# Kernel optimization log

Hardware: AMD Instinct MI355X
Metric: run time of the kernel (lower is better)

The kernel has to match this reference:

```python
import jax, jax.numpy as jnp
import numpy as np

DIM, HEAD, FFN = 256, 4, 1024
NEG = -1e9


def layer_norm(x, g, b, eps=1e-5):
    mu = jnp.mean(x, axis=-1, keepdims=True)
    var = jnp.mean((x - mu) ** 2, axis=-1, keepdims=True)
    return (x - mu) / jnp.sqrt(var + eps) * g + b


def setup_inputs() -> dict:
    key = jax.random.key(0)
    ks = jax.random.split(key, 10)
    B, T, D = 8, 2048, DIM
    s = 1.0 / np.sqrt(D)
    x = jax.random.normal(ks[0], (B, T, D), dtype=jnp.float32)
    mask = jax.random.randint(ks[1], (B, T), 0, 2).astype(jnp.float32)
    Wqkv = jax.random.uniform(ks[2], (3 * D, D), jnp.float32, -s, s)
    bqkv = jnp.zeros((3 * D,), jnp.float32)
    Wo = jax.random.uniform(ks[3], (D, D), jnp.float32, -s, s)
    bo = jnp.zeros((D,), jnp.float32)
    W1 = jax.random.uniform(ks[4], (FFN, D), jnp.float32, -s, s)
    b1 = jnp.zeros((FFN,), jnp.float32)
    W2 = jax.random.uniform(ks[5], (D, FFN), jnp.float32, -1.0 / np.sqrt(FFN), 1.0 / np.sqrt(FFN))
    b2 = jnp.zeros((D,), jnp.float32)
    g1 = jnp.ones((D,), jnp.float32); be1 = jnp.zeros((D,), jnp.float32)
    g2 = jnp.ones((D,), jnp.float32); be2 = jnp.zeros((D,), jnp.float32)
    return dict(x=x, mask=mask, Wqkv=Wqkv, bqkv=bqkv, Wo=Wo, bo=bo,
                W1=W1, b1=b1, W2=W2, b2=b2, g1=g1, be1=be1, g2=g2, be2=be2)


def _forward(x, mask, Wqkv, bqkv, Wo, bo, W1, b1, W2, b2, g1, be1, g2, be2):
    B, T, D = x.shape
    H = HEAD
    hd = D // H
    # --- MultiheadAttention (explicit, non-flash path, need_weights=True) ---
    qkv = jnp.einsum('btd,ed->bte', x, Wqkv) + bqkv            # (B,T,3D)
    q, k, v = jnp.split(qkv, 3, axis=-1)
    q = q.reshape(B, T, H, hd).transpose(0, 2, 1, 3)           # (B,H,T,hd)
    k = k.reshape(B, T, H, hd).transpose(0, 2, 1, 3)
    v = v.reshape(B, T, H, hd).transpose(0, 2, 1, 3)
    scores = jnp.einsum('bhqd,bhkd->bhqk', q, k) / jnp.sqrt(jnp.float32(hd))
    scores = jnp.where(mask[:, None, None, :] > 0.5, NEG, scores)
    w = jax.nn.softmax(scores, axis=-1)                        # (B,H,T,T)
    attn = jnp.einsum('bhqk,bhkd->bhqd', w, v)                 # (B,H,T,hd)
    attn = attn.transpose(0, 2, 1, 3).reshape(B, T, D)
    attn_out = jnp.einsum('btd,ed->bte', attn, Wo) + bo        # (B,T,D)
    w_avg = jnp.mean(w, axis=1)                                # (B,T,T), averaged over heads
    # halting score: sum over query dim (dim=1), then masked softmax
    halting = jnp.sum(w_avg, axis=1)                           # (B,T)
    halting = jax.nn.softmax(halting + mask * (-1e10), axis=-1)
    # --- residual + LN + FFN + LN ---
    h = layer_norm(x + attn_out, g1, be1)
    ffn = jnp.einsum('btf,df->btd', jax.nn.relu(jnp.einsum('btd,fd->btf', h, W1) + b1), W2) + b2
    out = layer_norm(h + ffn, g2, be2)
    return out, halting


def reference(x, mask, Wqkv, bqkv, Wo, bo, W1, b1, W2, b2, g1, be1, g2, be2):
    return _forward(x, mask, Wqkv, bqkv, Wo, bo, W1, b1, W2, b2, g1, be1, g2, be2)
```

## Files before the change

### kernel.cpp

```cpp
#include <hip/hip_runtime.h>
#include <hip/hip_bf16.h>
#include <math.h>

namespace {

constexpr int B = 8, T = 2048, D = 256, H = 4, HD = 64, FF = 1024;
constexpr float QSCALE = 0.18033688f;

typedef __attribute__((ext_vector_type(8))) short short8;
typedef __attribute__((ext_vector_type(4))) short s16x4;
typedef __attribute__((ext_vector_type(4))) float f32x4;

__device__ __forceinline__ short f2bf(float f) {
    __hip_bfloat16 h = __float2bfloat16(f);
    return *reinterpret_cast<short*>(&h);
}
__device__ __forceinline__ float exp2a(float x) {
    float r; asm("v_exp_f32 %0, %1" : "=v"(r) : "v"(x)); return r;
}
__device__ __forceinline__ unsigned cvtpk(float lo, float hi) {
    unsigned r; asm("v_cvt_pk_bf16_f32 %0, %1, %2" : "=v"(r) : "v"(lo), "v"(hi)); return r;
}
__device__ __forceinline__ void gload16(const void* g, void* l) {
    __builtin_amdgcn_global_load_lds(
        (const __attribute__((address_space(1))) void*)g,
        (__attribute__((address_space(3))) void*)l, 16, 0, 0);
}

__global__ __launch_bounds__(256) void k_cvt(
        const float* __restrict__ x,  const float* __restrict__ wq,
        const float* __restrict__ wo, const float* __restrict__ w1,
        const float* __restrict__ w2,
        short* __restrict__ x16,  short* __restrict__ wq16,
        short* __restrict__ wo16, short* __restrict__ w116,
        short* __restrict__ w216) {
    const int N0 = 524288, N1 = 24576, N2 = 8192, N3 = 32768, N4 = 32768;
    const int total = N0 + N1 + N2 + N3 + N4;
    for (int i = blockIdx.x*256 + threadIdx.x; i < total; i += gridDim.x*256) {
        const float* s; short* d; int j = i;
        if (j < N0) { s = x; d = x16; }
        else { j -= N0;
            if (j < N1) { s = wq; d = wq16; }
            else { j -= N1;
                if (j < N2) { s = wo; d = wo16; }
                else { j -= N2;
                    if (j < N3) { s = w1; d = w116; }
                    else { j -= N3; s = w2; d = w216; }
                }
            }
        }
        float4 a = ((const float4*)s)[j*2], b2 = ((const float4*)s)[j*2+1];
        short8 o;
        o[0]=f2bf(a.x);  o[1]=f2bf(a.y);  o[2]=f2bf(a.z);  o[3]=f2bf(a.w);
        o[4]=f2bf(b2.x); o[5]=f2bf(b2.y); o[6]=f2bf(b2.z); o[7]=f2bf(b2.w);
        ((short8*)d)[j] = o;
    }
}

template<int MODE>
__global__ __launch_bounds__(256) void k_gemm128(
        const short* __restrict__ A, const short* __restrict__ W,
        const float* __restrict__ bias, const int K,
        short* __restrict__ oq, short* __restrict__ ok, short* __restrict__ ov,
        short* __restrict__ o16) {
    __shared__ char pool[34048];
    short* Asl = (short*)pool;
    short* Wsl = (short*)(pool + 16384);
    float (*Cs)[133] = (float(*)[133])pool;

    const int tid = threadIdx.x;
    const int w = tid >> 6, lane = tid & 63;
    const int qr = lane & 15, g = lane >> 4;
    const int wm = w >> 1, wn = w & 1;
    const int m0 = blockIdx.x * 128;
    const int n0 = blockIdx.y * 128;
    const int srow = lane >> 3;
    const int scb  = (lane & 7) ^ srow;

    f32x4 acc[4][4];
    #pragma unroll
    for (int i = 0; i < 4; i++)
        #pragma unroll
        for (int j = 0; j < 4; j++) acc[i][j] = (f32x4){0.f, 0.f, 0.f, 0.f};

    for (int k0 = 0; k0 < K; k0 += 64) {
        __syncthreads();
        #pragma unroll
        for (int i = 0; i < 4; i++) {
            const int chunk = i*4 + w;
            const int row = chunk*8 + srow;
            gload16(A + (size_t)(m0 + row)*K + k0 + scb*8, Asl + chunk*512);
            gload16(W + (size_t)(n0 + row)*K + k0 + scb*8, Wsl + chunk*512);
        }
        __syncthreads();
        #pragma unroll
        for (int kk = 0; kk < 2; kk++) {
            const int swz = ((g + 4*kk) ^ (qr & 7)) * 8;
            short8 af[4], bf[4];
            #pragma unroll
            for (int fm = 0; fm < 4; fm++)
                af[fm] = *(const short8*)(Asl + (wm*64 + fm*16 + qr)*64 + swz);
            #pragma unroll
            for (int fn = 0; fn < 4; fn++)
                bf[fn] = *(const short8*)(Wsl + (wn*64 + fn*16 + qr)*64 + swz);
            #pragma unroll
            for (int fm = 0; fm < 4; fm++)
                #pragma unroll
                for (int fn = 0; fn < 4; fn++)
                    acc[fm][fn] = __builtin_amdgcn_mfma_f32_16x16x32_bf16(
                        af[fm], bf[fn], acc[fm][fn], 0, 0, 0);
        }
    }

    const int b = m0 >> 11;
    const int tl0 = m0 & (T - 1);

    if (MODE == 0 && blockIdx.y >= 4) {
        #pragma unroll
        for (int fm = 0; fm < 4; fm++) {
            const int tl = tl0 + wm*64 + fm*16 + g*4;
            #pragma unroll
            for (int fn = 0; fn < 4; fn++) {
                const int nv = (n0 - 512) + wn*64 + fn*16 + qr;
                const int h = nv >> 6, d = nv & 63;
                const float bv = bias[n0 + wn*64 + fn*16 + qr];
                s16x4 pk;
                #pragma unroll
                for (int r = 0; r < 4; r++) pk[r] = f2bf(acc[fm][fn][r] + bv);
                *(s16x4*)&ov[((size_t)(b*H + h)*HD + d)*T + tl] = pk;
            }
        }
        return;
    }

    __syncthreads();
    const int erow = tid & 63, c0 = (tid >> 6) * 32;
    #pragma unroll
    for (int hh = 0; hh < 2; hh++) {
        if (wm == hh) {
            #pragma unroll
            for (int fm = 0; fm < 4; fm++)
                #pragma unroll
                for (int fn = 0; fn < 4; fn++)
                    #pragma unroll
                    for (int r = 0; r < 4; r++)
                        Cs[fm*16 + g*4 + r][wn*64 + fn*16 + qr] = acc[fm][fn][r];
        }
        __syncthreads();
        float vals[32];
        #pragma unroll
        for (int j = 0; j < 32; j++) vals[j] = Cs[erow][c0 + j] + bias[n0 + c0 + j];
        const int tl = tl0 + hh*64 + erow;
        if (MODE == 0) {
            const int by = blockIdx.y;
            short* dst = (by < 2) ? oq : ok;
            const float qs = (by < 2) ? QSCALE : 1.0f;
            const int h = (by & 1)*2 + (c0 >> 6);
            const int d0 = c0 & 63;
            short8 s0, s1, s2, s3;
            #pragma unroll
            for (int j = 0; j < 8; j++) {
                s0[j] = f2bf(vals[j]*qs);
                s1[j] = f2bf(vals[8+j]*qs);
                s2[j] = f2bf(vals[16+j]*qs);
                s3[j] = f2bf(vals[24+j]*qs);
            }
            short* p = dst + ((size_t)(b*H + h)*T + tl)*HD + d0;
            *(short8*)p = s0;
            *(short8*)(p + 8) = s1;
            *(short8*)(p + 16) = s2;
            *(short8*)(p + 24) = s3;
        } else {
            short8 s0, s1, s2, s3;
            #pragma unroll
            for (int j = 0; j < 8; j++) {
                s0[j] = f2bf(fmaxf(vals[j],    0.f));
                s1[j] = f2bf(fmaxf(vals[8+j],  0.f));
                s2[j] = f2bf(fmaxf(vals[16+j], 0.f));
                s3[j] = f2bf(fmaxf(vals[24+j], 0.f));
            }
            short* p = o16 + (size_t)(m0 + hh*64 + erow)*1024 + n0 + c0;
            *(short8*)p = s0;
            *(short8*)(p + 8) = s1;
            *(short8*)(p + 16) = s2;
            *(short8*)(p + 24) = s3;
        }
        if (hh == 0) __syncthreads();
    }
}

template<int MODE>
__global__ __launch_bounds__(256) void k_gemm(
        const short* __restrict__ A, const short* __restrict__ W,
        const float* __restrict__ bias, const int K,
        float* __restrict__ of) {
    __shared__ short As[64][72];
    __shared__ short Ws[64][72];
    __shared__ float Cs[64][68];
    const int tid = threadIdx.x;
    const int w = tid >> 6, lane = tid & 63;
    const int qr = lane & 15, g = lane >> 4;
    const int wm = w >> 1, wn = w & 1;
    const int m0 = blockIdx.x * 64;
    const int n0 = blockIdx.y * 64;
    const int srow = tid >> 2, scol = (tid & 3) * 8;
    const short* Ag = A + (size_t)(m0 + srow) * K + scol;
    const short* Wg = W + (size_t)(n0 + srow) * K + scol;

    f32x4 acc[2][2];
    #pragma unroll
    for (int i = 0; i < 2; i++)
        #pragma unroll
        for (int j = 0; j < 2; j++) acc[i][j] = (f32x4){0.f, 0.f, 0.f, 0.f};

    for (int k0 = 0; k0 < K; k0 += 64) {
        __syncthreads();
        *(short8*)&As[srow][scol]      = *(const short8*)(Ag + k0);
        *(short8*)&As[srow][scol + 32] = *(const short8*)(Ag + k0 + 32);
        *(short8*)&Ws[srow][scol]      = *(const short8*)(Wg + k0);
        *(short8*)&Ws[srow][scol + 32] = *(const short8*)(Wg + k0 + 32);
        __syncthreads();
        #pragma unroll
        for (int kk = 0; kk < 2; kk++) {
            short8 a0 = *(const short8*)&As[wm*32 + qr][g*8 + kk*32];
            short8 a1 = *(const short8*)&As[wm*32 + 16 + qr][g*8 + kk*32];
            short8 b0 = *(const short8*)&Ws[wn*32 + qr][g*8 + kk*32];
            short8 b1 = *(const short8*)&Ws[wn*32 + 16 + qr][g*8 + kk*32];
            acc[0][0] = __builtin_amdgcn_mfma_f32_16x16x32_bf16(a0, b0, acc[0][0], 0, 0, 0);
            acc[0][1] = __builtin_amdgcn_mfma_f32_16x16x32_bf16(a0, b1, acc[0][1], 0, 0, 0);
            acc[1][0] = __builtin_amdgcn_mfma_f32_16x16x32_bf16(a1, b0, acc[1][0], 0, 0, 0);
            acc[1][1] = __builtin_amdgcn_mfma_f32_16x16x32_bf16(a1, b1, acc[1][1], 0, 0, 0);
        }
    }

    #pragma unroll
    for (int fm = 0; fm < 2; fm++)
        #pragma unroll
        for (int fn = 0; fn < 2; fn++)
            #pragma unroll
            for (int r = 0; r < 4; r++)
                Cs[wm*32 + fm*16 + g*4 + r][wn*32 + fn*16 + qr] = acc[fm][fn][r];
    __syncthreads();
    const int row = tid >> 2, c0 = (tid & 3) * 16;
    float vals[16];
    #pragma unroll
    for (int j = 0; j < 16; j++) vals[j] = Cs[row][c0 + j] + bias[n0 + c0 + j];
    float* p = of + (size_t)(m0 + row)*256 + n0 + c0;
    #pragma unroll
    for (int jj = 0; jj < 4; jj++) *(float4*)(p + jj*4) = *(float4*)&vals[jj*4];
}

__global__ __launch_bounds__(256) void k_flashL(
        const short* __restrict__ qb, const short* __restrict__ kb,
        const float* __restrict__ mask, float* __restrict__ liout) {
    __shared__ short Ks[128][72];
    __shared__ float lbuf[4][4][16];
    const int tid = threadIdx.x;
    const int w = tid >> 6, lane = tid & 63;
    const int qr = lane & 15, g = lane >> 4;
    const int qt = blockIdx.x, h = blockIdx.y, b = blockIdx.z;
    const int bh = b*H + h;
    const int q0 = qt*64;

    short8 qf[4][2];
    {
        const short* qg = qb + ((size_t)bh * T + q0) * HD;
        #pragma unroll
        for (int qt4 = 0; qt4 < 4; qt4++) {
            qf[qt4][0] = *(const short8*)(qg + (qt4*16 + qr)*HD + g*8);
            qf[qt4][1] = *(const short8*)(qg + (qt4*16 + qr)*HD + 32 + g*8);
        }
    }
    const short* kg0 = kb + (size_t)bh * T * HD;
    const float* mg  = mask + (size_t)b * T;
    const int krow = lane >> 1, khalf = (lane & 1) * 32;

    float lrun[4] = {0.f, 0.f, 0.f, 0.f};

    short8 kreg[4];
    #pragma unroll
    for (int c = 0; c < 4; c++)
        kreg[c] = *(const short8*)(kg0 + (size_t)(w*32 + krow)*HD + khalf + c*8);
    #pragma unroll
    for (int c = 0; c < 4; c++)
        *(short8*)&Ks[w*32 + krow][khalf + c*8] = kreg[c];
    asm volatile("" ::: "memory");

    for (int kt = 0; kt < 16; kt++) {
        const int kbase = kt*128 + w*32;
        if (kt < 15) {
            const int nb = (kt+1)*128 + w*32;
            #pragma unroll
            for (int c = 0; c < 4; c++)
                kreg[c] = *(const short8*)(kg0 + (size_t)(nb + krow)*HD + khalf + c*8);
        }
        #pragma unroll
        for (int kt2 = 0; kt2 < 2; kt2++) {
            short8 kf0 = *(const short8*)&Ks[w*32 + kt2*16 + qr][g*8];
            short8 kf1 = *(const short8*)&Ks[w*32 + kt2*16 + qr][g*8 + 32];
            const int key0 = kbase + kt2*16;
            const float4 mv4 = *(const float4*)(mg + key0 + 4*g);
            const float b0 = (mv4.x > 0.5f) ? -1e9f : 0.f;
            const float b1 = (mv4.y > 0.5f) ? -1e9f : 0.f;
            const float b2v = (mv4.z > 0.5f) ? -1e9f : 0.f;
            const float b3 = (mv4.w > 0.5f) ? -1e9f : 0.f;
            #pragma unroll
            for (int qt4 = 0; qt4 < 4; qt4++) {
                f32x4 sa = (f32x4){b0, b1, b2v, b3};
                sa = __builtin_amdgcn_mfma_f32_16x16x32_bf16(kf0, qf[qt4][0], sa, 0, 0, 0);
                sa = __builtin_amdgcn_mfma_f32_16x16x32_bf16(kf1, qf[qt4][1], sa, 0, 0, 0);
                lrun[qt4] += (exp2a(sa[0]) + exp2a(sa[1])) + (exp2a(sa[2]) + exp2a(sa[3]));
            }
        }
        if (kt < 15) {
            asm volatile("" ::: "memory");
            #pragma unroll
            for (int c = 0; c < 4; c++)
                *(short8*)&Ks[w*32 + krow][khalf + c*8] = kreg[c];
            asm volatile("" ::: "memory");
        }
    }
    #pragma unroll
    for (int qt4 = 0; qt4 < 4; qt4++) {
        lrun[qt4] += __shfl_xor(lrun[qt4], 16, 64);
        lrun[qt4] += __shfl_xor(lrun[qt4], 32, 64);
    }
    if (g == 0) {
        #pragma unroll
        for (int qt4 = 0; qt4 < 4; qt4++) lbuf[w][qt4][qr] = lrun[qt4];
    }
    __syncthreads();
    if (tid < 64) {
        const int qt4 = tid >> 4, qrr = tid & 15;
        const float l = lbuf[0][qt4][qrr] + lbuf[1][qt4][qrr]
                      + lbuf[2][qt4][qrr] + lbuf[3][qt4][qrr];
        liout[(size_t)bh*T + q0 + tid] = -__log2f(l);
    }
}

__global__ __launch_bounds__(256) void k_fattn(
        const short* __restrict__ qb, const short* __restrict__ kb,
        const short* __restrict__ vtb, const float* __restrict__ mask,
        const float* __restrict__ liout,
        short* __restrict__ attnb, float* __restrict__ part4) {
    __shared__ short Ks[128][68];
    __shared__ short Vt[64][132];
    __shared__ short Ps[4][64][36];
    const int tid = threadIdx.x;
    const int w = tid >> 6, lane = tid & 63;
    const int qr = lane & 15, g = lane >> 4;
    const int qt = blockIdx.x, h = blockIdx.y, b = blockIdx.z;
    const int bh = b*H + h;
    const int q0 = qt*64;

    short8 qf[4][2];
    float li[4];
    {
        const short* qg = qb + ((size_t)bh * T + q0) * HD;
        #pragma unroll
        for (int qt4 = 0; qt4 < 4; qt4++) {
            qf[qt4][0] = *(const short8*)(qg + (qt4*16 + qr)*HD + g*8);
            qf[qt4][1] = *(const short8*)(qg + (qt4*16 + qr)*HD + 32 + g*8);
            li[qt4] = liout[(size_t)bh*T + q0 + qt4*16 + qr];
        }
    }
    const short* kg0 = kb + (size_t)bh * T * HD;
    const short* vg0 = vtb + (size_t)bh * HD * T;
    const float* mg  = mask + (size_t)b * T;
    float* csrow = part4 + (size_t)(bh*32 + qt) * T;
    const int krow = lane >> 1, khalf = (lane & 1) * 32;

    f32x4 oa[4][4];
    #pragma unroll
    for (int nt = 0; nt < 4; nt++)
        #pragma unroll
        for (int qt4 = 0; qt4 < 4; qt4++) oa[nt][qt4] = (f32x4){0.f,0.f,0.f,0.f};

    short8 kreg[4], vreg[4];
    #pragma unroll
    for (int c = 0; c < 4; c++) {
        kreg[c] = *(const short8*)(kg0 + (size_t)(w*32 + krow)*HD + khalf + c*8);
        vreg[c] = *(const short8*)(vg0 + (size_t)lane*T + w*32 + c*8);
    }
    #pragma unroll
    for (int c = 0; c < 4; c++) {
        *(short8*)&Ks[w*32 + krow][khalf + c*8] = kreg[c];
        *(short8*)&Vt[lane][w*32 + c*8] = vreg[c];
    }
    asm volatile("" ::: "memory");

    for (int kt = 0; kt < 16; kt++) {
        if (kt < 15) {
            const int nb = (kt+1)*128 + w*32;
            #pragma unroll
            for (int c = 0; c < 4; c++) {
                kreg[c] = *(const short8*)(kg0 + (size_t)(nb + krow)*HD + khalf + c*8);
                vreg[c] = *(const short8*)(vg0 + (size_t)lane*T + nb + c*8);
            }
        }
        const int kbase = kt*128 + w*32;
        #pragma unroll
        for (int kt2 = 0; kt2 < 2; kt2++) {
            short8 kf0 = *(const short8*)&Ks[w*32 + kt2*16 + qr][g*8];
            short8 kf1 = *(const short8*)&Ks[w*32 + kt2*16 + qr][g*8 + 32];
            const int key0 = kbase + kt2*16;
            const float4 mv4 = *(const float4*)(mg + key0 + 4*g);
            const float mb[4] = { (mv4.x > 0.5f) ? -1e9f : 0.f,
                                  (mv4.y > 0.5f) ? -1e9f : 0.f,
                                  (mv4.z > 0.5f) ? -1e9f : 0.f,
                                  (mv4.w > 0.5f) ? -1e9f : 0.f };
            float p[4][4];
            #pragma unroll
            for (int qt4 = 0; qt4 < 4; qt4++) {
                f32x4 sa = (f32x4){mb[0] + li[qt4], mb[1] + li[qt4],
                                   mb[2] + li[qt4], mb[3] + li[qt4]};
                sa = __builtin_amdgcn_mfma_f32_16x16x32_bf16(kf0, qf[qt4][0], sa, 0, 0, 0);
                sa = __builtin_amdgcn_mfma_f32_16x16x32_bf16(kf1, qf[qt4][1], sa, 0, 0, 0);
                p[qt4][0] = exp2a(sa[0]); p[qt4][1] = exp2a(sa[1]);
                p[qt4][2] = exp2a(sa[2]); p[qt4][3] = exp2a(sa[3]);
            }
            float cs[4];
            #pragma unroll
            for (int r = 0; r < 4; r++) {
                cs[r] = (p[0][r] + p[1][r]) + (p[2][r] + p[3][r]);
                cs[r] += __shfl_xor(cs[r], 1, 64);
                cs[r] += __shfl_xor(cs[r], 2, 64);
                cs[r] += __shfl_xor(cs[r], 4, 64);
                cs[r] += __shfl_xor(cs[r], 8, 64);
            }
            if (qr == 0) {
                #pragma unroll
                for (int r = 0; r < 4; r++) csrow[key0 + 4*g + r] = cs[r];
            }
            #pragma unroll
            for (int qt4 = 0; qt4 < 4; qt4++) {
                union { unsigned u[2]; s16x4 s; } cv;
                cv.u[0] = cvtpk(p[qt4][0], p[qt4][1]);
                cv.u[1] = cvtpk(p[qt4][2], p[qt4][3]);
                *(s16x4*)&Ps[w][qt4*16 + qr][kt2*16 + 4*g] = cv.s;
            }
        }
        asm volatile("" ::: "memory");
        short8 pa[4];
        #pragma unroll
        for (int qt4 = 0; qt4 < 4; qt4++)
            pa[qt4] = *(const short8*)&Ps[w][qt4*16 + qr][g*8];
        #pragma unroll
        for (int nt = 0; nt < 4; nt++) {
            short8 vf = *(const short8*)&Vt[nt*16 + qr][w*32 + g*8];
            #pragma unroll
            for (int qt4 = 0; qt4 < 4; qt4++)
                oa[nt][qt4] = __builtin_amdgcn_mfma_f32_16x16x32_bf16(vf, pa[qt4], oa[nt][qt4], 0, 0, 0);
        }
        if (kt < 15) {
            asm volatile("" ::: "memory");
            #pragma unroll
            for (int c = 0; c < 4; c++) {
                *(short8*)&Ks[w*32 + krow][khalf + c*8] = kreg[c];
                *(short8*)&Vt[lane][w*32 + c*8] = vreg[c];
            }
            asm volatile("" ::: "memory");
        }
    }

    __syncthreads();
    float* Obuf = (float*)&Ks[0][0];
    const int qL = tid >> 2, dq = tid & 3;
    #pragma unroll
    for (int nt = 0; nt < 4; nt++) {
        #pragma unroll
        for (int qt4 = 0; qt4 < 4; qt4++)
            #pragma unroll
            for (int r = 0; r < 4; r++)
                Obuf[(w*16 + 4*g + r)*68 + qt4*16 + qr] = oa[nt][qt4][r];
        __syncthreads();
        s16x4 pk;
        #pragma unroll
        for (int rr = 0; rr < 4; rr++) {
            const int dr = dq*4 + rr;
            float v = Obuf[(0*16 + dr)*68 + qL] + Obuf[(1*16 + dr)*68 + qL]
                    + Obuf[(2*16 + dr)*68 + qL] + Obuf[(3*16 + dr)*68 + qL];
            pk[rr] = f2bf(v);
        }
        *(s16x4*)&attnb[((size_t)b*T + q0 + qL)*D + h*HD + nt*16 + dq*4] = pk;
        __syncthreads();
    }
}

__global__ __launch_bounds__(256) void k_red(
        const float* __restrict__ part, float* __restrict__ red) {
    __shared__ float s[128];
    const int b = blockIdx.y, kc = blockIdx.x;
    const int tid = threadIdx.x;
    const int c = tid & 127, half = tid >> 7;
    const int k = kc*128 + c;
    const float* pb = part + ((size_t)(b*128 + half*64))*T + k;
    float acc = 0.f;
    #pragma unroll 8
    for (int r = 0; r < 64; r++) acc += pb[(size_t)r*T];
    if (half) s[c] = acc;
    __syncthreads();
    if (!half) red[(size_t)b*T + k] = acc + s[c];
}

__global__ __launch_bounds__(256) void k_halt(
        const float* __restrict__ red, const float* __restrict__ mask,
        float* __restrict__ outh) {
    __shared__ float redm[4], reds[4];
    const int b = blockIdx.x, tid = threadIdx.x;
    const float* mg = mask + (size_t)b * T;
    float v[8];
    float M = -3e38f;
    #pragma unroll
    for (int i = 0; i < 8; i++) {
        v[i] = red[(size_t)b*T + tid + i*256]*0.25f + mg[tid + i*256]*(-1e10f);
        M = fmaxf(M, v[i]);
    }
    #pragma unroll
    for (int off = 1; off < 64; off <<= 1) M = fmaxf(M, __shfl_xor(M, off, 64));
    const int wv = tid >> 6, lane = tid & 63;
    if (lane == 0) redm[wv] = M;
    __syncthreads();
    M = fmaxf(fmaxf(redm[0], redm[1]), fmaxf(redm[2], redm[3]));
    float S = 0.f;
    #pragma unroll
    for (int i = 0; i < 8; i++) { v[i] = __expf(v[i] - M); S += v[i]; }
    #pragma unroll
    for (int off = 1; off < 64; off <<= 1) S += __shfl_xor(S, off, 64);
    if (lane == 0) reds[wv] = S;
    __syncthreads();
    const float invS = 1.f / (reds[0] + reds[1] + reds[2] + reds[3]);
    #pragma unroll
    for (int i = 0; i < 8; i++) outh[(size_t)b*T + tid + i*256] = v[i]*invS;
}

__global__ __launch_bounds__(256) void k_ln(
        const float* __restrict__ a, const float* __restrict__ bsrc,
        const float* __restrict__ g, const float* __restrict__ be,
        float* __restrict__ yf, short* __restrict__ y16) {
    __shared__ float s[16][D];
    const int tid = threadIdx.x;
    const size_t row0 = (size_t)blockIdx.x * 16;
    const float4* ag = (const float4*)(a + row0*D);
    const float4* bg = (const float4*)(bsrc + row0*D);
    #pragma unroll
    for (int i = 0; i < 4; i++) {
        float4 av = ag[tid + i*256], bv = bg[tid + i*256];
        float4 sv = {av.x+bv.x, av.y+bv.y, av.z+bv.z, av.w+bv.w};
        ((float4*)&s[0][0])[tid + i*256] = sv;
    }
    __syncthreads();
    const int wv = tid >> 6, lane = tid & 63;
    float gvv[4], bvv[4];
    #pragma unroll
    for (int s2 = 0; s2 < 4; s2++) { gvv[s2] = g[lane + 64*s2]; bvv[s2] = be[lane + 64*s2]; }
    #pragma unroll
    for (int rr = 0; rr < 4; rr++) {
        const int r = wv*4 + rr;
        float x0 = s[r][lane],     x1 = s[r][lane+64];
        float x2 = s[r][lane+128], x3 = s[r][lane+192];
        float sum = x0+x1+x2+x3;
        float ssq = x0*x0 + x1*x1 + x2*x2 + x3*x3;
        #pragma unroll
        for (int off = 1; off < 64; off <<= 1) {
            sum += __shfl_xor(sum, off, 64);
            ssq += __shfl_xor(ssq, off, 64);
        }
        const float mu = sum * (1.f/256.f);
        const float rs = rsqrtf(ssq*(1.f/256.f) - mu*mu + 1e-5f);
        float y0 = (x0 - mu)*rs*gvv[0] + bvv[0];
        float y1 = (x1 - mu)*rs*gvv[1] + bvv[1];
        float y2 = (x2 - mu)*rs*gvv[2] + bvv[2];
        float y3 = (x3 - mu)*rs*gvv[3] + bvv[3];
        float* yp = yf + (row0 + r)*D;
        yp[lane]     = y0;
        yp[lane+64]  = y1;
        yp[lane+128] = y2;
        yp[lane+192] = y3;
        if (y16) {
            short* hp = y16 + (row0 + r)*D;
            hp[lane]     = f2bf(y0);
            hp[lane+64]  = f2bf(y1);
            hp[lane+128] = f2bf(y2);
            hp[lane+192] = f2bf(y3);
        }
    }
}

}

extern "C" void kernel_launch(void* const* d_in, const int* in_sizes, int n_in,
                              void* d_out, int out_size, void* d_ws, size_t ws_size,
                              hipStream_t stream) {
    (void)in_sizes; (void)n_in; (void)out_size; (void)ws_size;
    const float* x    = (const float*)d_in[0];
    const float* mask = (const float*)d_in[1];
    const float* Wqkv = (const float*)d_in[2];
    const float* bqkv = (const float*)d_in[3];
    const float* Wo   = (const float*)d_in[4];
    const float* bo   = (const float*)d_in[5];
    const float* W1   = (const float*)d_in[6];
    const float* b1   = (const float*)d_in[7];
    const float* W2   = (const float*)d_in[8];
    const float* b2   = (const float*)d_in[9];
    const float* g1   = (const float*)d_in[10];
    const float* be1  = (const float*)d_in[11];
    const float* g2   = (const float*)d_in[12];
    const float* be2  = (const float*)d_in[13];

    float* out  = (float*)d_out;
    char*  wsb  = (char*)d_ws;
    const size_t MB = 1024*1024;

    short* qb16   = (short*)(wsb + 0*MB);
    short* kb16   = (short*)(wsb + 8*MB);
    short* vt16   = (short*)(wsb + 16*MB);
    short* x16    = (short*)(wsb + 24*MB);
    short* attn16 = (short*)(wsb + 24*MB);
    short* mid16  = (short*)(wsb + 0*MB);
    float* part4  = (float*)(wsb + 32*MB);
    float* redb   = (float*)(wsb + 40*MB);
    float* liout  = (float*)(wsb + 41*MB);
    short* wq16   = (short*)(wsb + 42*MB);
    short* wo16   = (short*)(wsb + 42*MB + 393216);
    short* w116   = (short*)(wsb + 42*MB + 524288);
    short* w216   = (short*)(wsb + 42*MB + 1048576);
    float* hb     = (float*)(wsb + 44*MB);
    short* h16    = (short*)(wsb + 60*MB);
    float* po     = (float*)(wsb + 68*MB);
    float* fo     = (float*)(wsb + 68*MB);
    float* outh   = out + (size_t)B*T*D;

    k_cvt      <<<dim3(1024),       256, 0, stream>>>(x, Wqkv, Wo, W1, W2,
                                                      x16, wq16, wo16, w116, w216);
    k_gemm128<0><<<dim3(128, 6),    256, 0, stream>>>(x16, wq16, bqkv, 256,
                                                      qb16, kb16, vt16, nullptr);
    k_flashL   <<<dim3(32, H, B),   256, 0, stream>>>(qb16, kb16, mask, liout);
    k_fattn    <<<dim3(32, H, B),   256, 0, stream>>>(qb16, kb16, vt16, mask, liout,
                                                      attn16, part4);
    k_red      <<<dim3(16, B),      256, 0, stream>>>(part4, redb);
    k_halt     <<<dim3(B),          256, 0, stream>>>(redb, mask, outh);
    k_gemm<1>  <<<dim3(256, 4),     256, 0, stream>>>(attn16, wo16, bo, 256, po);
    k_ln       <<<dim3(B*T/16),     256, 0, stream>>>(x, po, g1, be1, hb, h16);
    k_gemm128<2><<<dim3(128, 8),    256, 0, stream>>>(h16, w116, b1, 256,
                                                      nullptr, nullptr, nullptr, mid16);
    k_gemm<3>  <<<dim3(256, 4),     256, 0, stream>>>(mid16, w216, b2, 1024, fo);
    k_ln       <<<dim3(B*T/16),     256, 0, stream>>>(hb, fo, g2, be2, out, nullptr);
}
```

Measured before the change: 231.9 us.

## Fuse softmax-denominator pass into attention kernel and use 128-tile GEMM for FFN2

Merges the separate row-sum (log-sum-exp) kernel into the attention kernel. Each block now computes its own denominators in a first pass over K, then runs the PV pass without a global round trip for liout and without a second launch. The second FFN GEMM also moves from the 64x64 kernel to the 128x128 tiled kernel through a new fp32 output mode. Risks are higher LDS use and register pressure in the fused attention kernel, and fewer blocks (256) for the FFN2 GEMM.

```diff
diff --git a/kernel.cpp b/kernel.cpp
--- a/kernel.cpp
+++ b/kernel.cpp
@@ -62,7 +62,7 @@
         const short* __restrict__ A, const short* __restrict__ W,
         const float* __restrict__ bias, const int K,
         short* __restrict__ oq, short* __restrict__ ok, short* __restrict__ ov,
-        short* __restrict__ o16) {
+        short* __restrict__ o16, float* __restrict__ ofp) {
     __shared__ char pool[34048];
     short* Asl = (short*)pool;
     short* Wsl = (short*)(pool + 16384);
@@ -170,7 +170,7 @@
             *(short8*)(p + 8) = s1;
             *(short8*)(p + 16) = s2;
             *(short8*)(p + 24) = s3;
-        } else {
+        } else if (MODE == 2) {
             short8 s0, s1, s2, s3;
             #pragma unroll
             for (int j = 0; j < 8; j++) {
@@ -184,6 +184,11 @@
             *(short8*)(p + 8) = s1;
             *(short8*)(p + 16) = s2;
             *(short8*)(p + 24) = s3;
+        } else {
+            float* p = ofp + (size_t)(m0 + hh*64 + erow)*256 + n0 + c0;
+            #pragma unroll
+            for (int jj = 0; jj < 8; jj++)
+                *(float4*)(p + jj*4) = *(float4*)&vals[jj*4];
         }
         if (hh == 0) __syncthreads();
     }
@@ -250,10 +255,13 @@
     for (int jj = 0; jj < 4; jj++) *(float4*)(p + jj*4) = *(float4*)&vals[jj*4];
 }
 
-__global__ __launch_bounds__(256) void k_flashL(
+__global__ __launch_bounds__(256) void k_flatt(
         const short* __restrict__ qb, const short* __restrict__ kb,
-        const float* __restrict__ mask, float* __restrict__ liout) {
-    __shared__ short Ks[128][72];
+        const short* __restrict__ vtb, const float* __restrict__ mask,
+        short* __restrict__ attnb, float* __restrict__ part4) {
+    __shared__ short Ks[128][68];
+    __shared__ short Vt[64][132];
+    __shared__ short Ps[4][64][36];
     __shared__ float lbuf[4][4][16];
     const int tid = threadIdx.x;
     const int w = tid >> 6, lane = tid & 63;
@@ -272,103 +280,75 @@
         }
     }
     const short* kg0 = kb + (size_t)bh * T * HD;
-    const float* mg  = mask + (size_t)b * T;
-    const int krow = lane >> 1, khalf = (lane & 1) * 32;
-
-    float lrun[4] = {0.f, 0.f, 0.f, 0.f};
-
-    short8 kreg[4];
-    #pragma unroll
-    for (int c = 0; c < 4; c++)
-        kreg[c] = *(const short8*)(kg0 + (size_t)(w*32 + krow)*HD + khalf + c*8);
-    #pragma unroll
-    for (int c = 0; c < 4; c++)
-        *(short8*)&Ks[w*32 + krow][khalf + c*8] = kreg[c];
-    asm volatile("" ::: "memory");
-
-    for (int kt = 0; kt < 16; kt++) {
-        const int kbase = kt*128 + w*32;
-        if (kt < 15) {
-            const int nb = (kt+1)*128 + w*32;
-            #pragma unroll
-            for (int c = 0; c < 4; c++)
-                kreg[c] = *(const short8*)(kg0 + (size_t)(nb + krow)*HD + khalf + c*8);
-        }
-        #pragma unroll
-        for (int kt2 = 0; kt2 < 2; kt2++) {
-            short8 kf0 = *(const short8*)&Ks[w*32 + kt2*16 + qr][g*8];
-            short8 kf1 = *(const short8*)&Ks[w*32 + kt2*16 + qr][g*8 + 32];
-            const int key0 = kbase + kt2*16;
-            const float4 mv4 = *(const float4*)(mg + key0 + 4*g);
-            const float b0 = (mv4.x > 0.5f) ? -1e9f : 0.f;
-            const float b1 = (mv4.y > 0.5f) ? -1e9f : 0.f;
-            const float b2v = (mv4.z > 0.5f) ? -1e9f : 0.f;
-            const float b3 = (mv4.w > 0.5f) ? -1e9f : 0.f;
-            #pragma unroll
-            for (int qt4 = 0; qt4 < 4; qt4++) {
-                f32x4 sa = (f32x4){b0, b1, b2v, b3};
-                sa = __builtin_amdgcn_mfma_f32_16x16x32_bf16(kf0, qf[qt4][0], sa, 0, 0, 0);
-                sa = __builtin_amdgcn_mfma_f32_16x16x32_bf16(kf1, qf[qt4][1], sa, 0, 0, 0);
-                lrun[qt4] += (exp2a(sa[0]) + exp2a(sa[1])) + (exp2a(sa[2]) + exp2a(sa[3]));
-            }
-        }
-        if (kt < 15) {
-            asm volatile("" ::: "memory");
-            #pragma unroll
-            for (int c = 0; c < 4; c++)
-                *(short8*)&Ks[w*32 + krow][khalf + c*8] = kreg[c];
-            asm volatile("" ::: "memory");
-        }
-    }
-    #pragma unroll
-    for (int qt4 = 0; qt4 < 4; qt4++) {
-        lrun[qt4] += __shfl_xor(lrun[qt4], 16, 64);
-        lrun[qt4] += __shfl_xor(lrun[qt4], 32, 64);
-    }
-    if (g == 0) {
-        #pragma unroll
-        for (int qt4 = 0; qt4 < 4; qt4++) lbuf[w][qt4][qr] = lrun[qt4];
-    }
-    __syncthreads();
-    if (tid < 64) {
-        const int qt4 = tid >> 4, qrr = tid & 15;
-        const float l = lbuf[0][qt4][qrr] + lbuf[1][qt4][qrr]
-                      + lbuf[2][qt4][qrr] + lbuf[3][qt4][qrr];
-        liout[(size_t)bh*T + q0 + tid] = -__log2f(l);
-    }
-}
-
-__global__ __launch_bounds__(256) void k_fattn(
-        const short* __restrict__ qb, const short* __restrict__ kb,
-        const short* __restrict__ vtb, const float* __restrict__ mask,
-        const float* __restrict__ liout,
-        short* __restrict__ attnb, float* __restrict__ part4) {
-    __shared__ short Ks[128][68];
-    __shared__ short Vt[64][132];
-    __shared__ short Ps[4][64][36];
-    const int tid = threadIdx.x;
-    const int w = tid >> 6, lane = tid & 63;
-    const int qr = lane & 15, g = lane >> 4;
-    const int qt = blockIdx.x, h = blockIdx.y, b = blockIdx.z;
-    const int bh = b*H + h;
-    const int q0 = qt*64;
-
-    short8 qf[4][2];
-    float li[4];
-    {
-        const short* qg = qb + ((size_t)bh * T + q0) * HD;
-        #pragma unroll
-        for (int qt4 = 0; qt4 < 4; qt4++) {
-            qf[qt4][0] = *(const short8*)(qg + (qt4*16 + qr)*HD + g*8);
-            qf[qt4][1] = *(const short8*)(qg + (qt4*16 + qr)*HD + 32 + g*8);
-            li[qt4] = liout[(size_t)bh*T + q0 + qt4*16 + qr];
-        }
-    }
-    const short* kg0 = kb + (size_t)bh * T * HD;
     const short* vg0 = vtb + (size_t)bh * HD * T;
     const float* mg  = mask + (size_t)b * T;
     float* csrow = part4 + (size_t)(bh*32 + qt) * T;
     const int krow = lane >> 1, khalf = (lane & 1) * 32;
+
+    float lrun[4] = {0.f, 0.f, 0.f, 0.f};
+    {
+        short8 kreg[4];
+        #pragma unroll
+        for (int c = 0; c < 4; c++)
+            kreg[c] = *(const short8*)(kg0 + (size_t)(w*32 + krow)*HD + khalf + c*8);
+        #pragma unroll
+        for (int c = 0; c < 4; c++)
+            *(short8*)&Ks[w*32 + krow][khalf + c*8] = kreg[c];
+        asm volatile("" ::: "memory");
+
+        for (int kt = 0; kt < 16; kt++) {
+            const int kbase = kt*128 + w*32;
+            if (kt < 15) {
+                const int nb = (kt+1)*128 + w*32;
+                #pragma unroll
+                for (int c = 0; c < 4; c++)
+                    kreg[c] = *(const short8*)(kg0 + (size_t)(nb + krow)*HD + khalf + c*8);
+            }
+            #pragma unroll
+            for (int kt2 = 0; kt2 < 2; kt2++) {
+                short8 kf0 = *(const short8*)&Ks[w*32 + kt2*16 + qr][g*8];
+                short8 kf1 = *(const short8*)&Ks[w*32 + kt2*16 + qr][g*8 + 32];
+                const int key0 = kbase + kt2*16;
+                const float4 mv4 = *(const float4*)(mg + key0 + 4*g);
+                const float b0 = (mv4.x > 0.5f) ? -1e9f : 0.f;
+                const float b1 = (mv4.y > 0.5f) ? -1e9f : 0.f;
+                const float b2v = (mv4.z > 0.5f) ? -1e9f : 0.f;
+                const float b3 = (mv4.w > 0.5f) ? -1e9f : 0.f;
+                #pragma unroll
+                for (int qt4 = 0; qt4 < 4; qt4++) {
+                    f32x4 sa = (f32x4){b0, b1, b2v, b3};
+                    sa = __builtin_amdgcn_mfma_f32_16x16x32_bf16(kf0, qf[qt4][0], sa, 0, 0, 0);
+                    sa = __builtin_amdgcn_mfma_f32_16x16x32_bf16(kf1, qf[qt4][1], sa, 0, 0, 0);
+                    lrun[qt4] += (exp2a(sa[0]) + exp2a(sa[1])) + (exp2a(sa[2]) + exp2a(sa[3]));
+                }
+            }
+            if (kt < 15) {
+                asm volatile("" ::: "memory");
+                #pragma unroll
+                for (int c = 0; c < 4; c++)
+                    *(short8*)&Ks[w*32 + krow][khalf + c*8] = kreg[c];
+                asm volatile("" ::: "memory");
+            }
+        }
+    }
+    #pragma unroll
+    for (int qt4 = 0; qt4 < 4; qt4++) {
+        lrun[qt4] += __shfl_xor(lrun[qt4], 16, 64);
+        lrun[qt4] += __shfl_xor(lrun[qt4], 32, 64);
+    }
+    if (g == 0) {
+        #pragma unroll
+        for (int qt4 = 0; qt4 < 4; qt4++) lbuf[w][qt4][qr] = lrun[qt4];
+    }
+    __syncthreads();
+    float li[4];
+    #pragma unroll
+    for (int qt4 = 0; qt4 < 4; qt4++) {
+        const float l = lbuf[0][qt4][qr] + lbuf[1][qt4][qr]
+                      + lbuf[2][qt4][qr] + lbuf[3][qt4][qr];
+        li[qt4] = -__log2f(l);
+    }
+    __syncthreads();
 
     f32x4 oa[4][4];
     #pragma unroll
@@ -620,7 +600,6 @@
     short* mid16  = (short*)(wsb + 0*MB);
     float* part4  = (float*)(wsb + 32*MB);
     float* redb   = (float*)(wsb + 40*MB);
-    float* liout  = (float*)(wsb + 41*MB);
     short* wq16   = (short*)(wsb + 42*MB);
     short* wo16   = (short*)(wsb + 42*MB + 393216);
     short* w116   = (short*)(wsb + 42*MB + 524288);
@@ -634,16 +613,16 @@
     k_cvt      <<<dim3(1024),       256, 0, stream>>>(x, Wqkv, Wo, W1, W2,
                                                       x16, wq16, wo16, w116, w216);
     k_gemm128<0><<<dim3(128, 6),    256, 0, stream>>>(x16, wq16, bqkv, 256,
-                                                      qb16, kb16, vt16, nullptr);
-    k_flashL   <<<dim3(32, H, B),   256, 0, stream>>>(qb16, kb16, mask, liout);
-    k_fattn    <<<dim3(32, H, B),   256, 0, stream>>>(qb16, kb16, vt16, mask, liout,
+                                                      qb16, kb16, vt16, nullptr, nullptr);
+    k_flatt    <<<dim3(32, H, B),   256, 0, stream>>>(qb16, kb16, vt16, mask,
                                                       attn16, part4);
     k_red      <<<dim3(16, B),      256, 0, stream>>>(part4, redb);
     k_halt     <<<dim3(B),          256, 0, stream>>>(redb, mask, outh);
     k_gemm<1>  <<<dim3(256, 4),     256, 0, stream>>>(attn16, wo16, bo, 256, po);
     k_ln       <<<dim3(B*T/16),     256, 0, stream>>>(x, po, g1, be1, hb, h16);
     k_gemm128<2><<<dim3(128, 8),    256, 0, stream>>>(h16, w116, b1, 256,
-                                                      nullptr, nullptr, nullptr, mid16);
-    k_gemm<3>  <<<dim3(256, 4),     256, 0, stream>>>(mid16, w216, b2, 1024, fo);
+                                                      nullptr, nullptr, nullptr, mid16, nullptr);
+    k_gemm128<3><<<dim3(128, 2),    256, 0, stream>>>(mid16, w216, b2, 1024,
+                                                      nullptr, nullptr, nullptr, nullptr, fo);
     k_ln       <<<dim3(B*T/16),     256, 0, stream>>>(hb, fo, g2, be2, out, nullptr);
 }
```

Result: no change. 236.4 us (+1.9%).
